# Kernel optimization log

Measured on AMD Instinct MI355X. Metric: run time of the kernel, lower is better.

## Reference

```python
import jax, jax.numpy as jnp
import numpy as np

B, NX, NY, D_FEAT, CTX, S, T = 64, 32, 32, 1024, 512, 32, 4
N = NX * NY


def build_adjacency_matrix(nx, ny):
    # 4-neighborhood grid adjacency with self loops (faithful to original loop)
    adj = np.eye(nx * ny, dtype=np.float32)
    row = 0
    for i in range(nx):
        for j in range(ny):
            if i > 0:
                adj[row, j + (i - 1) * nx] = 1.0
            if i < nx - 1:
                adj[row, j + (i + 1) * nx] = 1.0
            if j > 0:
                adj[row, j - 1 + i * nx] = 1.0
            if j < ny - 1:
                adj[row, j + 1 + i * nx] = 1.0
            row += 1
    return adj


def setup_inputs() -> dict:
    key = jax.random.key(0)
    ks = jax.random.split(key, 12)
    s = 0.02
    return {
        "images": jax.random.normal(ks[0], (B, N, D_FEAT), jnp.float32),
        "q_encoding": jax.random.normal(ks[1], (B, CTX), jnp.float32),
        "lstm_outputs": jax.random.normal(ks[2], (B, S, CTX), jnp.float32),
        "q_length": jax.random.randint(ks[3], (B,), 1, S + 1, jnp.int32),
        "adj": jnp.asarray(build_adjacency_matrix(NX, NY)),
        "initKB_w": jax.random.normal(ks[4], (CTX, D_FEAT), jnp.float32) * s,
        "initKB_b": jnp.zeros((CTX,), jnp.float32),
        "W_w": jax.random.normal(ks[5], (CTX, 2 * CTX), jnp.float32) * s,
        "W_b": jnp.zeros((CTX,), jnp.float32),
        "qInput_w": jax.random.normal(ks[6], (CTX, CTX), jnp.float32) * s,
        "qInput_b": jnp.zeros((CTX,), jnp.float32),
        "qInputT_w": jax.random.normal(ks[7], (T, CTX, CTX), jnp.float32) * s,
        "qInputT_b": jnp.zeros((T, CTX), jnp.float32),
        "cmd_w": jax.random.normal(ks[8], (1, CTX), jnp.float32) * s,
        "cmd_b": jnp.zeros((1,), jnp.float32),
    }


def reference(images, q_encoding, lstm_outputs, q_length, adj,
              initKB_w, initKB_b, W_w, W_b, qInput_w, qInput_b,
              qInputT_w, qInputT_b, cmd_w, cmd_b) -> jnp.ndarray:
    n_iter = qInputT_w.shape[0]
    seq = lstm_outputs.shape[1]
    # loc_init: images [B,N,D_FEAT] -> x_loc [B,N,CTX]
    x_loc = jnp.einsum("bnd,cd->bnc", images, initKB_w) + initKB_b
    # shared first command layer (cfg.CMD_INPUT_ACT = elu)
    q1 = jax.nn.elu(q_encoding @ qInput_w.T + qInput_b)  # [B,CTX]
    valid = jnp.arange(seq)[None, :] < q_length[:, None]  # [B,S]
    for t in range(n_iter):
        # extract_textual_command
        q_cmd = q1 @ qInputT_w[t].T + qInputT_b[t]  # [B,CTX]
        raw_att = jnp.einsum("bsd,d->bs", q_cmd[:, None, :] * lstm_outputs, cmd_w[0]) + cmd_b[0]
        raw_att = jnp.where(valid, raw_att, -1e30)
        att = jax.nn.softmax(raw_att, axis=-1)  # [B,S]
        cmd = jnp.einsum("bs,bsd->bd", att, lstm_outputs)  # [B,CTX]
        # propagate_message: concat + linear, then dense adjacency matmul
        cmd_tiled = jnp.broadcast_to(cmd[:, None, :], x_loc.shape)
        support = jnp.concatenate([x_loc, cmd_tiled], axis=-1) @ W_w.T + W_b  # [B,N,CTX]
        x_new = jnp.einsum("nm,bmd->bnd", adj, support)  # [B,N,CTX]
        x_loc = jax.nn.elu(x_new) if t < n_iter - 1 else x_new
    return x_loc
```

## Files before the change

### kernel.cpp

```cpp
#include <hip/hip_runtime.h>
#include <hip/hip_bf16.h>
#include <math.h>

#define NB 64
#define NNODES 1024
#define CTXD 512
#define SEQL 32

typedef __attribute__((ext_vector_type(8))) short short8;
typedef __attribute__((ext_vector_type(4))) float floatx4;

__device__ __forceinline__ float bf2f(unsigned short u) {
  union { unsigned int i; float f; } v; v.i = ((unsigned int)u) << 16; return v.f;
}
__device__ __forceinline__ unsigned short f2bf(float f) {
  union { float f; unsigned int i; } v; v.f = f;
  unsigned int r = v.i + 0x7fffu + ((v.i >> 16) & 1u);
  return (unsigned short)(r >> 16);
}
__device__ __forceinline__ float elu1(float x) { return x > 0.f ? x : expm1f(x); }

__device__ __forceinline__ void gload16(const void* g, void* l) {
  __builtin_amdgcn_global_load_lds((const __attribute__((address_space(1))) void*)g,
                                   (__attribute__((address_space(3))) void*)l, 16, 0, 0);
}

__global__ __launch_bounds__(256) void pack_k(const float* __restrict__ kbw,
                                              const float* __restrict__ Ww,
                                              const float* __restrict__ qiw,
                                              const float* __restrict__ qtw,
                                              unsigned short* __restrict__ kb_bf,
                                              unsigned short* __restrict__ w1_bf,
                                              float* __restrict__ qiT,
                                              float* __restrict__ qTT,
                                              float* __restrict__ w2T) {
  int idx = blockIdx.x * 256 + threadIdx.x;
  if (idx < 524288) {
    kb_bf[idx] = f2bf(kbw[idx]);
  } else if (idx < 786432) {
    int o = idx - 524288;
    w1_bf[o] = f2bf(Ww[(o >> 9) * 1024 + (o & 511)]);
  } else if (idx < 1048576) {
    int o = idx - 786432;
    int k = o >> 9, c = o & 511;
    qiT[o] = qiw[c * 512 + k];
  } else if (idx < 2097152) {
    int o = idx - 1048576;
    int t = o >> 18, r = o & 262143;
    int k = r >> 9, c = r & 511;
    qTT[o] = qtw[((size_t)t * 512 + c) * 512 + k];
  } else {
    int o = idx - 2097152;
    int k = o >> 9, c = o & 511;
    w2T[o] = Ww[c * 1024 + 512 + k];
  }
}

__global__ __launch_bounds__(512) void q1_k(const float* __restrict__ q_enc,
                                            const float* __restrict__ qiT,
                                            const float* __restrict__ qInput_b,
                                            float* __restrict__ q1) {
  int b = blockIdx.x, c = threadIdx.x;
  __shared__ float qes[512];
  qes[c] = q_enc[b * 512 + c];
  __syncthreads();
  float a0 = qInput_b[c], a1 = 0.f, a2 = 0.f, a3 = 0.f;
#pragma unroll 4
  for (int k = 0; k < 512; k += 4) {
    a0 += qes[k] * qiT[k * 512 + c];
    a1 += qes[k + 1] * qiT[(k + 1) * 512 + c];
    a2 += qes[k + 2] * qiT[(k + 2) * 512 + c];
    a3 += qes[k + 3] * qiT[(k + 3) * 512 + c];
  }
  q1[b * 512 + c] = elu1(a0 + a1 + a2 + a3);
}

__global__ __launch_bounds__(512) void cmdt_k(
    const float* __restrict__ q1, const float* __restrict__ lstm,
    const int* __restrict__ q_len,
    const float* __restrict__ qTT, const float* __restrict__ qT_b,
    const float* __restrict__ cmd_w, const float* __restrict__ cmd_b,
    const float* __restrict__ w2T, const float* __restrict__ W_b,
    float* __restrict__ bias2) {
  int b = blockIdx.x & 63;
  int t = blockIdx.x >> 6;
  int c = threadIdx.x;
  __shared__ float q1s[512];
  __shared__ float us[512];
  __shared__ float red[512];
  __shared__ float atts[32];
  __shared__ float cmds[512];

  q1s[c] = q1[b * 512 + c];
  __syncthreads();

  const float* wt = qTT + (size_t)t * 262144;
  float a0 = qT_b[t * 512 + c], a1 = 0.f, a2 = 0.f, a3 = 0.f;
#pragma unroll 4
  for (int k = 0; k < 512; k += 4) {
    a0 += q1s[k] * wt[k * 512 + c];
    a1 += q1s[k + 1] * wt[(k + 1) * 512 + c];
    a2 += q1s[k + 2] * wt[(k + 2) * 512 + c];
    a3 += q1s[k + 3] * wt[(k + 3) * 512 + c];
  }
  us[c] = (a0 + a1 + a2 + a3) * cmd_w[c];
  __syncthreads();

  const float* lstmb = lstm + (size_t)b * SEQL * 512;
  {
    int s = c >> 4, u = c & 15;
    float p = 0.f;
    const float* lr = lstmb + s * 512;
    for (int r = u; r < 512; r += 16) p += us[r] * lr[r];
    red[c] = p;
  }
  __syncthreads();
  if (c < 32) {
    float raw = cmd_b[0];
    for (int u = 0; u < 16; u++) raw += red[c * 16 + u];
    raw = (c < q_len[b]) ? raw : -1e30f;
    float mx = raw;
    for (int off = 16; off; off >>= 1) mx = fmaxf(mx, __shfl_xor(mx, off, 32));
    float e = expf(raw - mx);
    float sm = e;
    for (int off = 16; off; off >>= 1) sm += __shfl_xor(sm, off, 32);
    atts[c] = e / sm;
  }
  __syncthreads();
  float cd = 0.f;
#pragma unroll
  for (int s = 0; s < 32; s++) cd += atts[s] * lstmb[s * 512 + c];
  cmds[c] = cd;
  __syncthreads();

  float b0 = W_b[c], b1 = 0.f, b2 = 0.f, b3 = 0.f;
#pragma unroll 4
  for (int k = 0; k < 512; k += 4) {
    b0 += cmds[k] * w2T[k * 512 + c];
    b1 += cmds[k + 1] * w2T[(k + 1) * 512 + c];
    b2 += cmds[k + 2] * w2T[(k + 2) * 512 + c];
    b3 += cmds[k + 3] * w2T[(k + 3) * 512 + c];
  }
  bias2[((size_t)(t * 64 + b)) * 512 + c] = b0 + b1 + b2 + b3;
}

__global__ __launch_bounds__(256) void stencil_k(const unsigned short* __restrict__ x,
                                                 unsigned short* __restrict__ y) {
  int g = blockIdx.x * 256 + threadIdx.x;
  int v = g & 63;
  int n = (g >> 6) & 1023;
  int b = g >> 16;
  size_t base = ((((size_t)b << 10) + n) << 9) + v * 8;
  const unsigned short* p = x + base;
  float acc[8];
  short8 s = *(const short8*)p;
#pragma unroll
  for (int j = 0; j < 8; j++) acc[j] = bf2f((unsigned short)s[j]);
  int i = n >> 5, jj = n & 31;
  if (i > 0) {
    short8 t = *(const short8*)(p - 32 * 512);
#pragma unroll
    for (int j = 0; j < 8; j++) acc[j] += bf2f((unsigned short)t[j]);
  }
  if (i < 31) {
    short8 t = *(const short8*)(p + 32 * 512);
#pragma unroll
    for (int j = 0; j < 8; j++) acc[j] += bf2f((unsigned short)t[j]);
  }
  if (jj > 0) {
    short8 t = *(const short8*)(p - 512);
#pragma unroll
    for (int j = 0; j < 8; j++) acc[j] += bf2f((unsigned short)t[j]);
  }
  if (jj < 31) {
    short8 t = *(const short8*)(p + 512);
#pragma unroll
    for (int j = 0; j < 8; j++) acc[j] += bf2f((unsigned short)t[j]);
  }
  short8 o;
#pragma unroll
  for (int j = 0; j < 8; j++) o[j] = (short)f2bf(acc[j]);
  *(short8*)(y + base) = o;
}

__global__ __launch_bounds__(256, 4) void igemm(
    const float* __restrict__ Af,
    const unsigned short* __restrict__ Bw,
    const float* __restrict__ cbias,
    unsigned short* __restrict__ Cp) {
  __shared__ __align__(128) unsigned short As[64 * 64];
  __shared__ __align__(128) unsigned short Bs[256 * 64];

  const int tid = threadIdx.x;
  const int lane = tid & 63;
  const int wn = tid >> 6;
  const int lr = lane & 15;
  const int lk = lane >> 4;
  const int lr7 = lr & 7;

  int bid = blockIdx.x;
  int wg = (bid & 7) * (gridDim.x >> 3) + (bid >> 3);
  const size_t rowBase = (size_t)(wg >> 1) * 64;
  const int colBase = (wg & 1) * 256;

  floatx4 acc[4][4];
#pragma unroll
  for (int m = 0; m < 4; m++)
#pragma unroll
    for (int n = 0; n < 4; n++) acc[m][n] = {0.f, 0.f, 0.f, 0.f};

  for (int k0 = 0; k0 < 1024; k0 += 64) {
    __syncthreads();
#pragma unroll
    for (int j = 0; j < 2; j++) {
      int g = j * 256 + tid;
      int r = g >> 3, u = g & 7;
      const float* src = Af + (rowBase + r) * (size_t)1024 + k0 + u * 8;
      floatx4 v0 = *(const floatx4*)src;
      floatx4 v1 = *(const floatx4*)(src + 4);
      short8 t;
#pragma unroll
      for (int e = 0; e < 4; e++) {
        t[e] = (short)f2bf(v0[e]);
        t[e + 4] = (short)f2bf(v1[e]);
      }
      *(short8*)((char*)As + r * 128 + ((u ^ (r & 7)) << 4)) = t;
    }
#pragma unroll
    for (int j = 0; j < 8; j++) {
      int g = j * 256 + tid;
      int r = g >> 3, u = g & 7;
      gload16(Bw + (size_t)(colBase + r) * 1024 + k0 + ((u ^ (r & 7)) << 3),
              (char*)Bs + g * 16);
    }
    __syncthreads();

#pragma unroll
    for (int kk = 0; kk < 2; kk++) {
      const int ub = ((kk << 2) + lk) ^ lr7;
      short8 a[4], b[4];
#pragma unroll
      for (int m = 0; m < 4; m++)
        a[m] = *(const short8*)((const char*)As + (m * 16 + lr) * 128 + (ub << 4));
#pragma unroll
      for (int n = 0; n < 4; n++)
        b[n] = *(const short8*)((const char*)Bs + (wn * 64 + n * 16 + lr) * 128 + (ub << 4));
#pragma unroll
      for (int m = 0; m < 4; m++)
#pragma unroll
        for (int n = 0; n < 4; n++)
          acc[m][n] = __builtin_amdgcn_mfma_f32_16x16x32_bf16(a[m], b[n], acc[m][n], 0, 0, 0);
    }
  }

#pragma unroll
  for (int m = 0; m < 4; m++) {
#pragma unroll
    for (int q = 0; q < 4; q++) {
      size_t grow = rowBase + m * 16 + lk * 4 + q;
#pragma unroll
      for (int n = 0; n < 4; n++) {
        int gcol = colBase + wn * 64 + n * 16 + lr;
        Cp[grow * CTXD + gcol] = f2bf(acc[m][n][q] + cbias[gcol]);
      }
    }
  }
}

template <int MODE>
__global__ __launch_bounds__(512, 2) void gemm8(
    const unsigned short* __restrict__ Ay,
    const unsigned short* __restrict__ Bw,
    const float* __restrict__ bias2,
    void* __restrict__ Cp) {
  __shared__ __align__(128) unsigned short AsL[2][2][8192];
  __shared__ __align__(128) unsigned short BsL[2][2][8192];

  const int tid = threadIdx.x;
  const int lane = tid & 63;
  const int wave = tid >> 6;
  const int wm = wave >> 2;
  const int wn = wave & 3;
  const int lr = lane & 15;
  const int lk = lane >> 4;
  const int lr7 = lr & 7;
  const int rB0 = (wn & 1) * 64;

  int bid = blockIdx.x;
  int wg = (bid & 7) * (gridDim.x >> 3) + (bid >> 3);
  const size_t rowBase = (size_t)(wg >> 1) * 256;
  const int colBase = (wg & 1) * 256;

  floatx4 acc[8][4];
#pragma unroll
  for (int m = 0; m < 8; m++)
#pragma unroll
    for (int n = 0; n < 4; n++) acc[m][n] = {0.f, 0.f, 0.f, 0.f};

  auto stgA = [&](int d, int h, int kt) {
#pragma unroll
    for (int j = 0; j < 2; j++) {
      int g = j * 512 + tid, r = g >> 3, u = g & 7;
      gload16(Ay + (rowBase + h * 128 + r) * (size_t)512 + kt * 64 + ((u ^ (r & 7)) << 3),
              (char*)&AsL[d][h][0] + g * 16);
    }
  };
  auto stgB = [&](int d, int h, int kt) {
#pragma unroll
    for (int j = 0; j < 2; j++) {
      int g = j * 512 + tid, r = g >> 3, u = g & 7;
      gload16(Bw + (size_t)(colBase + h * 128 + r) * 512 + kt * 64 + ((u ^ (r & 7)) << 3),
              (char*)&BsL[d][h][0] + g * 16);
    }
  };

  stgB(0, 0, 0); stgA(0, 0, 0); stgA(0, 1, 0); stgB(0, 1, 0);
  stgB(1, 0, 1); stgA(1, 0, 1);
  asm volatile("s_waitcnt vmcnt(4)" ::: "memory");
  __builtin_amdgcn_sched_barrier(0);
  __builtin_amdgcn_s_barrier();
  __builtin_amdgcn_sched_barrier(0);

  short8 a[2][4], b[2][4];

  for (int t = 0; t < 8; t++) {
    const int d = t & 1;
    const char* Ah = (const char*)&AsL[d][wm][0];
    const char* Bh = (const char*)&BsL[d][wn >> 1][0];

#pragma unroll
    for (int kk = 0; kk < 2; kk++) {
      const int ub = ((kk << 2) + lk) ^ lr7;
#pragma unroll
      for (int m = 0; m < 4; m++)
        a[kk][m] = *(const short8*)(Ah + (m * 16 + lr) * 128 + (ub << 4));
#pragma unroll
      for (int n = 0; n < 2; n++)
        b[kk][n] = *(const short8*)(Bh + (rB0 + n * 16 + lr) * 128 + (ub << 4));
    }
    if (t + 1 < 8) stgA(d ^ 1, 1, t + 1);
    __builtin_amdgcn_sched_barrier(0);
    __builtin_amdgcn_s_barrier();
    asm volatile("s_waitcnt lgkmcnt(0)" ::: "memory");
    __builtin_amdgcn_sched_barrier(0);
    __builtin_amdgcn_s_setprio(1);
#pragma unroll
    for (int kk = 0; kk < 2; kk++)
#pragma unroll
      for (int m = 0; m < 4; m++)
#pragma unroll
        for (int n = 0; n < 2; n++)
          acc[m][n] = __builtin_amdgcn_mfma_f32_16x16x32_bf16(a[kk][m], b[kk][n], acc[m][n], 0, 0, 0);
    __builtin_amdgcn_s_setprio(0);
    __builtin_amdgcn_sched_barrier(0);
    __builtin_amdgcn_s_barrier();
    __builtin_amdgcn_sched_barrier(0);

#pragma unroll
    for (int kk = 0; kk < 2; kk++) {
      const int ub = ((kk << 2) + lk) ^ lr7;
#pragma unroll
      for (int n = 2; n < 4; n++)
        b[kk][n] = *(const short8*)(Bh + (rB0 + n * 16 + lr) * 128 + (ub << 4));
    }
    if (t + 1 < 8) stgB(d ^ 1, 1, t + 1);
    __builtin_amdgcn_sched_barrier(0);
    __builtin_amdgcn_s_barrier();
    asm volatile("s_waitcnt lgkmcnt(0)" ::: "memory");
    __builtin_amdgcn_sched_barrier(0);
    __builtin_amdgcn_s_setprio(1);
#pragma unroll
    for (int kk = 0; kk < 2; kk++)
#pragma unroll
      for (int m = 0; m < 4; m++)
#pragma unroll
        for (int n = 2; n < 4; n++)
          acc[m][n] = __builtin_amdgcn_mfma_f32_16x16x32_bf16(a[kk][m], b[kk][n], acc[m][n], 0, 0, 0);
    __builtin_amdgcn_s_setprio(0);
    __builtin_amdgcn_sched_barrier(0);
    __builtin_amdgcn_s_barrier();
    __builtin_amdgcn_sched_barrier(0);

#pragma unroll
    for (int kk = 0; kk < 2; kk++) {
      const int ub = ((kk << 2) + lk) ^ lr7;
#pragma unroll
      for (int m = 0; m < 4; m++)
        a[kk][m] = *(const short8*)(Ah + (64 + m * 16 + lr) * 128 + (ub << 4));
    }
    if (t + 2 < 8) stgB(d, 0, t + 2);
    __builtin_amdgcn_sched_barrier(0);
    __builtin_amdgcn_s_barrier();
    asm volatile("s_waitcnt lgkmcnt(0)" ::: "memory");
    __builtin_amdgcn_sched_barrier(0);
    __builtin_amdgcn_s_setprio(1);
#pragma unroll
    for (int kk = 0; kk < 2; kk++)
#pragma unroll
      for (int m = 0; m < 4; m++)
#pragma unroll
        for (int n = 0; n < 2; n++)
          acc[m + 4][n] = __builtin_amdgcn_mfma_f32_16x16x32_bf16(a[kk][m], b[kk][n], acc[m + 4][n], 0, 0, 0);
    __builtin_amdgcn_s_setprio(0);
    __builtin_amdgcn_sched_barrier(0);
    __builtin_amdgcn_s_barrier();
    __builtin_amdgcn_sched_barrier(0);

    if (t + 2 < 8) stgA(d, 0, t + 2);
    __builtin_amdgcn_sched_barrier(0);
    __builtin_amdgcn_s_setprio(1);
#pragma unroll
    for (int kk = 0; kk < 2; kk++)
#pragma unroll
      for (int m = 0; m < 4; m++)
#pragma unroll
        for (int n = 2; n < 4; n++)
          acc[m + 4][n] = __builtin_amdgcn_mfma_f32_16x16x32_bf16(a[kk][m], b[kk][n], acc[m + 4][n], 0, 0, 0);
    __builtin_amdgcn_s_setprio(0);
    __builtin_amdgcn_sched_barrier(0);
    if (t + 2 < 8) {
      asm volatile("s_waitcnt vmcnt(4)" ::: "memory");
    } else {
      asm volatile("s_waitcnt vmcnt(0)" ::: "memory");
    }
    __builtin_amdgcn_sched_barrier(0);
    __builtin_amdgcn_s_barrier();
    __builtin_amdgcn_sched_barrier(0);
  }

#pragma unroll
  for (int m = 0; m < 8; m++) {
#pragma unroll
    for (int q = 0; q < 4; q++) {
      size_t grow = rowBase + wm * 128 + m * 16 + lk * 4 + q;
      int nsp = (int)(grow & 1023);
      int ii = nsp >> 5, jj = nsp & 31;
      float degf = (float)(1 + (ii > 0) + (ii < 31) + (jj > 0) + (jj < 31));
      const float* b2 = bias2 + (grow >> 10) * CTXD;
#pragma unroll
      for (int n = 0; n < 4; n++) {
        int gcol = colBase + wn * 64 + n * 16 + lr;
        float v = acc[m][n][q] + degf * b2[gcol];
        if constexpr (MODE == 1) {
          ((unsigned short*)Cp)[grow * CTXD + gcol] = f2bf(elu1(v));
        } else {
          ((float*)Cp)[grow * CTXD + gcol] = v;
        }
      }
    }
  }
}

extern "C" void kernel_launch(void* const* d_in, const int* in_sizes, int n_in,
                              void* d_out, int out_size, void* d_ws, size_t ws_size,
                              hipStream_t stream) {
  const float* images   = (const float*)d_in[0];
  const float* q_enc    = (const float*)d_in[1];
  const float* lstm     = (const float*)d_in[2];
  const int*   q_len    = (const int*)d_in[3];
  const float* initKB_w = (const float*)d_in[5];
  const float* initKB_b = (const float*)d_in[6];
  const float* W_w      = (const float*)d_in[7];
  const float* W_b      = (const float*)d_in[8];
  const float* qInput_w = (const float*)d_in[9];
  const float* qInput_b = (const float*)d_in[10];
  const float* qT_w     = (const float*)d_in[11];
  const float* qT_b     = (const float*)d_in[12];
  const float* cmd_w    = (const float*)d_in[13];
  const float* cmd_b    = (const float*)d_in[14];

  char* ws = (char*)d_ws;
  unsigned short* y     = (unsigned short*)ws;
  float*          qiT   = (float*)ws;
  float*          qTT   = (float*)(ws + 1048576);
  float*          w2T   = (float*)(ws + 5242880);
  unsigned short* kb_bf = (unsigned short*)(ws + 67108864);
  unsigned short* w1_bf = (unsigned short*)(ws + 68157440);
  float*          bias2 = (float*)(ws + 68681728);
  float*          q1    = (float*)(ws + 69206016);
  unsigned short* xloc  = (unsigned short*)d_out;

  pack_k<<<9216, 256, 0, stream>>>(initKB_w, W_w, qInput_w, qT_w,
                                   kb_bf, w1_bf, qiT, qTT, w2T);
  q1_k<<<64, 512, 0, stream>>>(q_enc, qiT, qInput_b, q1);
  cmdt_k<<<256, 512, 0, stream>>>(q1, lstm, q_len, qTT, qT_b, cmd_w, cmd_b,
                                  w2T, W_b, bias2);

  igemm<<<2048, 256, 0, stream>>>(images, kb_bf, initKB_b, xloc);

  for (int t = 0; t < 4; t++) {
    stencil_k<<<16384, 256, 0, stream>>>(xloc, y);
    if (t < 3)
      gemm8<1><<<512, 512, 0, stream>>>(y, w1_bf, bias2 + (size_t)t * 32768, xloc);
    else
      gemm8<2><<<512, 512, 0, stream>>>(y, w1_bf, bias2 + (size_t)t * 32768, d_out);
  }
}
```

Baseline: 531.9 us.

## Fold initKB projection into first propagation GEMM and fuse last stencil into GEMM

Precomputes W1·initKB_w as one weight matrix, plus W1·initKB_b folded into the first bias, so the image projection GEMM and the first message GEMM become a single K=1024 GEMM. The adjacency stencil is applied directly to the fp32 images before that GEMM. This removes one full B×N×512 GEMM and the intermediate x_loc round-trip. The final iteration uses a new fgemm kernel that gathers the stencil taps in its A-tile loader, which removes one stencil launch and its intermediate buffer. In exchange, the images stencil reads the larger 1024-wide fp32 tensor, and the prefolded weights are rounded to bf16, which changes the numerics.

```diff
diff --git a/kernel.cpp b/kernel.cpp
--- a/kernel.cpp
+++ b/kernel.cpp
@@ -8,6 +8,7 @@
 #define SEQL 32
 
 typedef __attribute__((ext_vector_type(8))) short short8;
+typedef __attribute__((ext_vector_type(4))) short short4v;
 typedef __attribute__((ext_vector_type(4))) float floatx4;
 
 __device__ __forceinline__ float bf2f(unsigned short u) {
@@ -25,34 +26,76 @@
                                    (__attribute__((address_space(3))) void*)l, 16, 0, 0);
 }
 
-__global__ __launch_bounds__(256) void pack_k(const float* __restrict__ kbw,
-                                              const float* __restrict__ Ww,
+__global__ __launch_bounds__(256) void pack_k(const float* __restrict__ Ww,
                                               const float* __restrict__ qiw,
                                               const float* __restrict__ qtw,
-                                              unsigned short* __restrict__ kb_bf,
                                               unsigned short* __restrict__ w1_bf,
                                               float* __restrict__ qiT,
                                               float* __restrict__ qTT,
                                               float* __restrict__ w2T) {
   int idx = blockIdx.x * 256 + threadIdx.x;
-  if (idx < 524288) {
-    kb_bf[idx] = f2bf(kbw[idx]);
-  } else if (idx < 786432) {
-    int o = idx - 524288;
-    w1_bf[o] = f2bf(Ww[(o >> 9) * 1024 + (o & 511)]);
-  } else if (idx < 1048576) {
-    int o = idx - 786432;
+  if (idx < 262144) {
+    w1_bf[idx] = f2bf(Ww[(idx >> 9) * 1024 + (idx & 511)]);
+  } else if (idx < 524288) {
+    int o = idx - 262144;
     int k = o >> 9, c = o & 511;
     qiT[o] = qiw[c * 512 + k];
-  } else if (idx < 2097152) {
-    int o = idx - 1048576;
+  } else if (idx < 1572864) {
+    int o = idx - 524288;
     int t = o >> 18, r = o & 262143;
     int k = r >> 9, c = r & 511;
     qTT[o] = qtw[((size_t)t * 512 + c) * 512 + k];
   } else {
-    int o = idx - 2097152;
+    int o = idx - 1572864;
     int k = o >> 9, c = o & 511;
     w2T[o] = Ww[c * 1024 + 512 + k];
+  }
+}
+
+__global__ __launch_bounds__(256) void w1kb_k(const float* __restrict__ Ww,
+                                              const float* __restrict__ kbw,
+                                              const float* __restrict__ ikb_b,
+                                              unsigned short* __restrict__ w1kb_bf,
+                                              float* __restrict__ w1b) {
+  int bi = blockIdx.x;
+  int tid = threadIdx.x;
+  if (bi == 128) {
+    __shared__ float bs[512];
+    bs[tid] = ikb_b[tid];
+    bs[tid + 256] = ikb_b[tid + 256];
+    __syncthreads();
+#pragma unroll
+    for (int rep = 0; rep < 2; rep++) {
+      int c = tid + rep * 256;
+      float s = 0.f;
+      for (int k = 0; k < 512; k++) s += Ww[(size_t)c * 1024 + k] * bs[k];
+      w1b[c] = s;
+    }
+    return;
+  }
+  __shared__ float ws1[4][512];
+  int cb = bi * 4;
+#pragma unroll
+  for (int e = 0; e < 8; e++) {
+    int o = e * 256 + tid;
+    ws1[o >> 9][o & 511] = Ww[(size_t)(cb + (o >> 9)) * 1024 + (o & 511)];
+  }
+  __syncthreads();
+  int d0 = tid * 4;
+  floatx4 a0 = {0.f, 0.f, 0.f, 0.f}, a1 = a0, a2 = a0, a3 = a0;
+  for (int c = 0; c < 512; c++) {
+    floatx4 kb = *(const floatx4*)&kbw[(size_t)c * 1024 + d0];
+    a0 += kb * ws1[0][c];
+    a1 += kb * ws1[1][c];
+    a2 += kb * ws1[2][c];
+    a3 += kb * ws1[3][c];
+  }
+#pragma unroll
+  for (int j = 0; j < 4; j++) {
+    w1kb_bf[(size_t)(cb + 0) * 1024 + d0 + j] = f2bf(a0[j]);
+    w1kb_bf[(size_t)(cb + 1) * 1024 + d0 + j] = f2bf(a1[j]);
+    w1kb_bf[(size_t)(cb + 2) * 1024 + d0 + j] = f2bf(a2[j]);
+    w1kb_bf[(size_t)(cb + 3) * 1024 + d0 + j] = f2bf(a3[j]);
   }
 }
 
@@ -81,6 +124,7 @@
     const float* __restrict__ qTT, const float* __restrict__ qT_b,
     const float* __restrict__ cmd_w, const float* __restrict__ cmd_b,
     const float* __restrict__ w2T, const float* __restrict__ W_b,
+    const float* __restrict__ w1b,
     float* __restrict__ bias2) {
   int b = blockIdx.x & 63;
   int t = blockIdx.x >> 6;
@@ -141,7 +185,29 @@
     b2 += cmds[k + 2] * w2T[(k + 2) * 512 + c];
     b3 += cmds[k + 3] * w2T[(k + 3) * 512 + c];
   }
-  bias2[((size_t)(t * 64 + b)) * 512 + c] = b0 + b1 + b2 + b3;
+  float res = b0 + b1 + b2 + b3;
+  if (t == 0) res += w1b[c];
+  bias2[((size_t)(t * 64 + b)) * 512 + c] = res;
+}
+
+__global__ __launch_bounds__(256) void stencil_img_k(const float* __restrict__ img,
+                                                     unsigned short* __restrict__ S) {
+  int g = blockIdx.x * 256 + threadIdx.x;
+  int v = g & 255;
+  int n = (g >> 8) & 1023;
+  int b = g >> 18;
+  size_t base = (((size_t)b * 1024 + n) * 1024) + v * 4;
+  const float* p = img + base;
+  floatx4 s = *(const floatx4*)p;
+  int i = n >> 5, j = n & 31;
+  if (i > 0)  s += *(const floatx4*)(p - 32 * 1024);
+  if (i < 31) s += *(const floatx4*)(p + 32 * 1024);
+  if (j > 0)  s += *(const floatx4*)(p - 1024);
+  if (j < 31) s += *(const floatx4*)(p + 1024);
+  short4v o;
+#pragma unroll
+  for (int e = 0; e < 4; e++) o[e] = (short)f2bf(s[e]);
+  *(short4v*)(S + base) = o;
 }
 
 __global__ __launch_bounds__(256) void stencil_k(const unsigned short* __restrict__ x,
@@ -183,91 +249,7 @@
   *(short8*)(y + base) = o;
 }
 
-__global__ __launch_bounds__(256, 4) void igemm(
-    const float* __restrict__ Af,
-    const unsigned short* __restrict__ Bw,
-    const float* __restrict__ cbias,
-    unsigned short* __restrict__ Cp) {
-  __shared__ __align__(128) unsigned short As[64 * 64];
-  __shared__ __align__(128) unsigned short Bs[256 * 64];
-
-  const int tid = threadIdx.x;
-  const int lane = tid & 63;
-  const int wn = tid >> 6;
-  const int lr = lane & 15;
-  const int lk = lane >> 4;
-  const int lr7 = lr & 7;
-
-  int bid = blockIdx.x;
-  int wg = (bid & 7) * (gridDim.x >> 3) + (bid >> 3);
-  const size_t rowBase = (size_t)(wg >> 1) * 64;
-  const int colBase = (wg & 1) * 256;
-
-  floatx4 acc[4][4];
-#pragma unroll
-  for (int m = 0; m < 4; m++)
-#pragma unroll
-    for (int n = 0; n < 4; n++) acc[m][n] = {0.f, 0.f, 0.f, 0.f};
-
-  for (int k0 = 0; k0 < 1024; k0 += 64) {
-    __syncthreads();
-#pragma unroll
-    for (int j = 0; j < 2; j++) {
-      int g = j * 256 + tid;
-      int r = g >> 3, u = g & 7;
-      const float* src = Af + (rowBase + r) * (size_t)1024 + k0 + u * 8;
-      floatx4 v0 = *(const floatx4*)src;
-      floatx4 v1 = *(const floatx4*)(src + 4);
-      short8 t;
-#pragma unroll
-      for (int e = 0; e < 4; e++) {
-        t[e] = (short)f2bf(v0[e]);
-        t[e + 4] = (short)f2bf(v1[e]);
-      }
-      *(short8*)((char*)As + r * 128 + ((u ^ (r & 7)) << 4)) = t;
-    }
-#pragma unroll
-    for (int j = 0; j < 8; j++) {
-      int g = j * 256 + tid;
-      int r = g >> 3, u = g & 7;
-      gload16(Bw + (size_t)(colBase + r) * 1024 + k0 + ((u ^ (r & 7)) << 3),
-              (char*)Bs + g * 16);
-    }
-    __syncthreads();
-
-#pragma unroll
-    for (int kk = 0; kk < 2; kk++) {
-      const int ub = ((kk << 2) + lk) ^ lr7;
-      short8 a[4], b[4];
-#pragma unroll
-      for (int m = 0; m < 4; m++)
-        a[m] = *(const short8*)((const char*)As + (m * 16 + lr) * 128 + (ub << 4));
-#pragma unroll
-      for (int n = 0; n < 4; n++)
-        b[n] = *(const short8*)((const char*)Bs + (wn * 64 + n * 16 + lr) * 128 + (ub << 4));
-#pragma unroll
-      for (int m = 0; m < 4; m++)
-#pragma unroll
-        for (int n = 0; n < 4; n++)
-          acc[m][n] = __builtin_amdgcn_mfma_f32_16x16x32_bf16(a[m], b[n], acc[m][n], 0, 0, 0);
-    }
-  }
-
-#pragma unroll
-  for (int m = 0; m < 4; m++) {
-#pragma unroll
-    for (int q = 0; q < 4; q++) {
-      size_t grow = rowBase + m * 16 + lk * 4 + q;
-#pragma unroll
-      for (int n = 0; n < 4; n++) {
-        int gcol = colBase + wn * 64 + n * 16 + lr;
-        Cp[grow * CTXD + gcol] = f2bf(acc[m][n][q] + cbias[gcol]);
-      }
-    }
-  }
-}
-
-template <int MODE>
+template <int MODE, int NT, int LDA, int LDB>
 __global__ __launch_bounds__(512, 2) void gemm8(
     const unsigned short* __restrict__ Ay,
     const unsigned short* __restrict__ Bw,
@@ -301,7 +283,7 @@
 #pragma unroll
     for (int j = 0; j < 2; j++) {
       int g = j * 512 + tid, r = g >> 3, u = g & 7;
-      gload16(Ay + (rowBase + h * 128 + r) * (size_t)512 + kt * 64 + ((u ^ (r & 7)) << 3),
+      gload16(Ay + (rowBase + h * 128 + r) * (size_t)LDA + kt * 64 + ((u ^ (r & 7)) << 3),
               (char*)&AsL[d][h][0] + g * 16);
     }
   };
@@ -309,7 +291,7 @@
 #pragma unroll
     for (int j = 0; j < 2; j++) {
       int g = j * 512 + tid, r = g >> 3, u = g & 7;
-      gload16(Bw + (size_t)(colBase + h * 128 + r) * 512 + kt * 64 + ((u ^ (r & 7)) << 3),
+      gload16(Bw + (size_t)(colBase + h * 128 + r) * LDB + kt * 64 + ((u ^ (r & 7)) << 3),
               (char*)&BsL[d][h][0] + g * 16);
     }
   };
@@ -323,7 +305,7 @@
 
   short8 a[2][4], b[2][4];
 
-  for (int t = 0; t < 8; t++) {
+  for (int t = 0; t < NT; t++) {
     const int d = t & 1;
     const char* Ah = (const char*)&AsL[d][wm][0];
     const char* Bh = (const char*)&BsL[d][wn >> 1][0];
@@ -338,7 +320,7 @@
       for (int n = 0; n < 2; n++)
         b[kk][n] = *(const short8*)(Bh + (rB0 + n * 16 + lr) * 128 + (ub << 4));
     }
-    if (t + 1 < 8) stgA(d ^ 1, 1, t + 1);
+    if (t + 1 < NT) stgA(d ^ 1, 1, t + 1);
     __builtin_amdgcn_sched_barrier(0);
     __builtin_amdgcn_s_barrier();
     asm volatile("s_waitcnt lgkmcnt(0)" ::: "memory");
@@ -363,7 +345,7 @@
       for (int n = 2; n < 4; n++)
         b[kk][n] = *(const short8*)(Bh + (rB0 + n * 16 + lr) * 128 + (ub << 4));
     }
-    if (t + 1 < 8) stgB(d ^ 1, 1, t + 1);
+    if (t + 1 < NT) stgB(d ^ 1, 1, t + 1);
     __builtin_amdgcn_sched_barrier(0);
     __builtin_amdgcn_s_barrier();
     asm volatile("s_waitcnt lgkmcnt(0)" ::: "memory");
@@ -388,7 +370,7 @@
       for (int m = 0; m < 4; m++)
         a[kk][m] = *(const short8*)(Ah + (64 + m * 16 + lr) * 128 + (ub << 4));
     }
-    if (t + 2 < 8) stgB(d, 0, t + 2);
+    if (t + 2 < NT) stgB(d, 0, t + 2);
     __builtin_amdgcn_sched_barrier(0);
     __builtin_amdgcn_s_barrier();
     asm volatile("s_waitcnt lgkmcnt(0)" ::: "memory");
@@ -406,7 +388,7 @@
     __builtin_amdgcn_s_barrier();
     __builtin_amdgcn_sched_barrier(0);
 
-    if (t + 2 < 8) stgA(d, 0, t + 2);
+    if (t + 2 < NT) stgA(d, 0, t + 2);
     __builtin_amdgcn_sched_barrier(0);
     __builtin_amdgcn_s_setprio(1);
 #pragma unroll
@@ -418,7 +400,7 @@
           acc[m + 4][n] = __builtin_amdgcn_mfma_f32_16x16x32_bf16(a[kk][m], b[kk][n], acc[m + 4][n], 0, 0, 0);
     __builtin_amdgcn_s_setprio(0);
     __builtin_amdgcn_sched_barrier(0);
-    if (t + 2 < 8) {
+    if (t + 2 < NT) {
       asm volatile("s_waitcnt vmcnt(4)" ::: "memory");
     } else {
       asm volatile("s_waitcnt vmcnt(0)" ::: "memory");
@@ -433,6 +415,177 @@
 #pragma unroll
     for (int q = 0; q < 4; q++) {
       size_t grow = rowBase + wm * 128 + m * 16 + lk * 4 + q;
+      int nsp = (int)(grow & 1023);
+      int ii = nsp >> 5, jj = nsp & 31;
+      float degf = (float)(1 + (ii > 0) + (ii < 31) + (jj > 0) + (jj < 31));
+      const float* b2 = bias2 + (grow >> 10) * CTXD;
+#pragma unroll
+      for (int n = 0; n < 4; n++) {
+        int gcol = colBase + wn * 64 + n * 16 + lr;
+        float v = acc[m][n][q] + degf * b2[gcol];
+        if constexpr (MODE == 1) {
+          ((unsigned short*)Cp)[grow * CTXD + gcol] = f2bf(elu1(v));
+        } else {
+          ((float*)Cp)[grow * CTXD + gcol] = v;
+        }
+      }
+    }
+  }
+}
+
+struct Taps { short8 c, up, dn, lf, rt; };
+
+template <int MODE>
+__global__ __launch_bounds__(512, 2) void fgemm(
+    const unsigned short* __restrict__ X,
+    const unsigned short* __restrict__ Bw,
+    const float* __restrict__ bias2,
+    void* __restrict__ Cp) {
+  __shared__ __align__(128) unsigned short AsL[2][128 * 64];
+  __shared__ __align__(128) unsigned short BsL[2][256 * 64];
+
+  const int tid = threadIdx.x;
+  const int lane = tid & 63;
+  const int wave = tid >> 6;
+  const int wm = wave >> 2;
+  const int wn = wave & 3;
+  const int lr = lane & 15;
+  const int lk = lane >> 4;
+  const int lr7 = lr & 7;
+
+  int bid = blockIdx.x;
+  int wg = (bid & 7) * (gridDim.x >> 3) + (bid >> 3);
+  const size_t rowBase = (size_t)(wg >> 1) * 128;
+  const int colBase = (wg & 1) * 256;
+
+  floatx4 acc[4][4];
+#pragma unroll
+  for (int m = 0; m < 4; m++)
+#pragma unroll
+    for (int n = 0; n < 4; n++) acc[m][n] = {0.f, 0.f, 0.f, 0.f};
+
+  const int rl = tid >> 3;
+  const int uu = tid & 7;
+
+  auto issueT = [&](Taps& T, int h, int kt) {
+    size_t R = rowBase + h * 64 + rl;
+    int n = (int)(R & 1023);
+    const unsigned short* p = X + R * 512 + kt * 64 + uu * 8;
+    T.c = *(const short8*)p;
+    T.up = *(const short8*)(p + (((n >> 5) > 0) ? -32 * 512 : 0));
+    T.dn = *(const short8*)(p + (((n >> 5) < 31) ? 32 * 512 : 0));
+    T.lf = *(const short8*)(p + (((n & 31) > 0) ? -512 : 0));
+    T.rt = *(const short8*)(p + (((n & 31) < 31) ? 512 : 0));
+  };
+  auto commitT = [&](const Taps& T, int h, int d) {
+    int r = h * 64 + rl;
+    size_t R = rowBase + r;
+    int n = (int)(R & 1023);
+    float mu = ((n >> 5) > 0) ? 1.f : 0.f;
+    float md = ((n >> 5) < 31) ? 1.f : 0.f;
+    float ml = ((n & 31) > 0) ? 1.f : 0.f;
+    float mr = ((n & 31) < 31) ? 1.f : 0.f;
+    short8 o;
+#pragma unroll
+    for (int e = 0; e < 8; e++) {
+      float s = bf2f((unsigned short)T.c[e]);
+      s += mu * bf2f((unsigned short)T.up[e]);
+      s += md * bf2f((unsigned short)T.dn[e]);
+      s += ml * bf2f((unsigned short)T.lf[e]);
+      s += mr * bf2f((unsigned short)T.rt[e]);
+      o[e] = (short)f2bf(s);
+    }
+    *(short8*)((char*)&AsL[d][0] + r * 128 + ((uu ^ (r & 7)) << 4)) = o;
+  };
+  auto stgB = [&](int d, int h, int kt) {
+#pragma unroll
+    for (int j = 0; j < 2; j++) {
+      int g = h * 1024 + j * 512 + tid;
+      int r = g >> 3, u = g & 7;
+      gload16(Bw + (size_t)(colBase + r) * 512 + kt * 64 + ((u ^ (r & 7)) << 3),
+              (char*)&BsL[d][0] + g * 16);
+    }
+  };
+  auto phase = [&](int d, int kk) {
+    const char* Ab = (const char*)&AsL[d][0];
+    const char* Bb = (const char*)&BsL[d][0];
+    const int ub = ((kk << 2) + lk) ^ lr7;
+    short8 a[4], b[4];
+#pragma unroll
+    for (int m = 0; m < 4; m++)
+      a[m] = *(const short8*)(Ab + (wm * 64 + m * 16 + lr) * 128 + (ub << 4));
+#pragma unroll
+    for (int n = 0; n < 4; n++)
+      b[n] = *(const short8*)(Bb + (wn * 64 + n * 16 + lr) * 128 + (ub << 4));
+    asm volatile("s_waitcnt lgkmcnt(0)" ::: "memory");
+    __builtin_amdgcn_sched_barrier(0);
+    __builtin_amdgcn_s_setprio(1);
+#pragma unroll
+    for (int m = 0; m < 4; m++)
+#pragma unroll
+      for (int n = 0; n < 4; n++)
+        acc[m][n] = __builtin_amdgcn_mfma_f32_16x16x32_bf16(a[m], b[n], acc[m][n], 0, 0, 0);
+    __builtin_amdgcn_s_setprio(0);
+    __builtin_amdgcn_sched_barrier(0);
+  };
+
+  Taps tH0, tH1;
+
+  issueT(tH0, 0, 0);
+  issueT(tH1, 1, 0);
+  __builtin_amdgcn_sched_barrier(0);
+  stgB(0, 0, 0);
+  stgB(0, 1, 0);
+  __builtin_amdgcn_sched_barrier(0);
+  asm volatile("s_waitcnt vmcnt(9)" ::: "memory");
+  __builtin_amdgcn_sched_barrier(0);
+  commitT(tH0, 0, 0);
+  asm volatile("s_waitcnt vmcnt(4)" ::: "memory");
+  __builtin_amdgcn_sched_barrier(0);
+  commitT(tH1, 1, 0);
+  issueT(tH0, 0, 1);
+  issueT(tH1, 1, 1);
+  __builtin_amdgcn_sched_barrier(0);
+  asm volatile("s_waitcnt vmcnt(10)" ::: "memory");
+  asm volatile("s_waitcnt lgkmcnt(0)" ::: "memory");
+  __builtin_amdgcn_sched_barrier(0);
+  __builtin_amdgcn_s_barrier();
+  __builtin_amdgcn_sched_barrier(0);
+
+  for (int t = 0; t < 8; t++) {
+    const int cur = t & 1, nxt = cur ^ 1;
+    const int ktn = (t + 1) & 7, kt2 = (t + 2) & 7;
+
+    stgB(nxt, 0, ktn);
+    __builtin_amdgcn_sched_barrier(0);
+    phase(cur, 0);
+    asm volatile("s_waitcnt vmcnt(7)" ::: "memory");
+    __builtin_amdgcn_sched_barrier(0);
+    commitT(tH0, 0, nxt);
+    __builtin_amdgcn_sched_barrier(0);
+
+    stgB(nxt, 1, ktn);
+    __builtin_amdgcn_sched_barrier(0);
+    phase(cur, 1);
+    asm volatile("s_waitcnt vmcnt(4)" ::: "memory");
+    __builtin_amdgcn_sched_barrier(0);
+    commitT(tH1, 1, nxt);
+    issueT(tH0, 0, kt2);
+    issueT(tH1, 1, kt2);
+    __builtin_amdgcn_sched_barrier(0);
+    asm volatile("s_waitcnt vmcnt(10)" ::: "memory");
+    asm volatile("s_waitcnt lgkmcnt(0)" ::: "memory");
+    __builtin_amdgcn_sched_barrier(0);
+    __builtin_amdgcn_s_barrier();
+    __builtin_amdgcn_sched_barrier(0);
+  }
+  asm volatile("s_waitcnt vmcnt(0)" ::: "memory");
+
+#pragma unroll
+  for (int m = 0; m < 4; m++) {
+#pragma unroll
+    for (int q = 0; q < 4; q++) {
+      size_t grow = rowBase + wm * 64 + m * 16 + lk * 4 + q;
       int nsp = (int)(grow & 1023);
       int ii = nsp >> 5, jj = nsp & 31;
       float degf = (float)(1 + (ii > 0) + (ii < 31) + (jj > 0) + (jj < 31));
@@ -470,29 +623,32 @@
   const float* cmd_b    = (const float*)d_in[14];
 
   char* ws = (char*)d_ws;
-  unsigned short* y     = (unsigned short*)ws;
-  float*          qiT   = (float*)ws;
-  float*          qTT   = (float*)(ws + 1048576);
-  float*          w2T   = (float*)(ws + 5242880);
-  unsigned short* kb_bf = (unsigned short*)(ws + 67108864);
-  unsigned short* w1_bf = (unsigned short*)(ws + 68157440);
-  float*          bias2 = (float*)(ws + 68681728);
-  float*          q1    = (float*)(ws + 69206016);
-  unsigned short* xloc  = (unsigned short*)d_out;
-
-  pack_k<<<9216, 256, 0, stream>>>(initKB_w, W_w, qInput_w, qT_w,
-                                   kb_bf, w1_bf, qiT, qTT, w2T);
+  unsigned short* X       = (unsigned short*)ws;
+  float*          qiT     = (float*)ws;
+  float*          qTT     = (float*)(ws + 1048576);
+  float*          w2T     = (float*)(ws + 5242880);
+  unsigned short* w1kb_bf = (unsigned short*)(ws + 67108864);
+  unsigned short* w1_bf   = (unsigned short*)(ws + 68157440);
+  float*          bias2   = (float*)(ws + 68681728);
+  float*          q1      = (float*)(ws + 69206016);
+  float*          w1b     = (float*)(ws + 69337088);
+  unsigned short* S       = (unsigned short*)d_out;
+  unsigned short* Y       = (unsigned short*)d_out;
+
+  pack_k<<<7168, 256, 0, stream>>>(W_w, qInput_w, qT_w, w1_bf, qiT, qTT, w2T);
+  w1kb_k<<<129, 256, 0, stream>>>(W_w, initKB_w, initKB_b, w1kb_bf, w1b);
   q1_k<<<64, 512, 0, stream>>>(q_enc, qiT, qInput_b, q1);
   cmdt_k<<<256, 512, 0, stream>>>(q1, lstm, q_len, qTT, qT_b, cmd_w, cmd_b,
-                                  w2T, W_b, bias2);
-
-  igemm<<<2048, 256, 0, stream>>>(images, kb_bf, initKB_b, xloc);
-
-  for (int t = 0; t < 4; t++) {
-    stencil_k<<<16384, 256, 0, stream>>>(xloc, y);
-    if (t < 3)
-      gemm8<1><<<512, 512, 0, stream>>>(y, w1_bf, bias2 + (size_t)t * 32768, xloc);
-    else
-      gemm8<2><<<512, 512, 0, stream>>>(y, w1_bf, bias2 + (size_t)t * 32768, d_out);
-  }
-}
+                                  w2T, W_b, w1b, bias2);
+
+  stencil_img_k<<<65536, 256, 0, stream>>>(images, S);
+
+  gemm8<1, 16, 1024, 1024><<<512, 512, 0, stream>>>(S, w1kb_bf, bias2, X);
+
+  stencil_k<<<16384, 256, 0, stream>>>(X, Y);
+  gemm8<1, 8, 512, 512><<<512, 512, 0, stream>>>(Y, w1_bf, bias2 + 32768, X);
+  stencil_k<<<16384, 256, 0, stream>>>(X, Y);
+  gemm8<1, 8, 512, 512><<<512, 512, 0, stream>>>(Y, w1_bf, bias2 + 2 * 32768, X);
+
+  fgemm<2><<<1024, 512, 0, stream>>>(X, w1_bf, bias2 + 3 * 32768, d_out);
+}
```

After: 648.0 us. 21.8% more time.
